# Performance work log

Measured on AMD Instinct MI355X. Metric: run time of the kernel, lower is better.

The kernel has to match this reference:

```python
import jax, jax.numpy as jnp
import numpy as np

N_NODES = 16384
N_EDGES = 524288
IN_CH = 128
HID_CH = 128
N_CLUST = 128


def _gcn_conv(x, W, b, src, dst, n):
    """PyG GCNConv: out = D^{-1/2} (A + I) D^{-1/2} (x @ W) + b, aggregating src -> dst."""
    h = x @ W  # [N, out]
    loop = jnp.arange(n)
    row = jnp.concatenate([src, loop])  # message sources (incl. self loops)
    col = jnp.concatenate([dst, loop])  # message targets
    deg = jax.ops.segment_sum(jnp.ones(row.shape, dtype=h.dtype), col, num_segments=n)
    dinv = jax.lax.rsqrt(deg)  # deg >= 1 thanks to self loops
    w = dinv[row] * dinv[col]  # [E + N]
    out = jax.ops.segment_sum(h[row] * w[:, None], col, num_segments=n)
    return out + b


def setup_inputs() -> dict:
    key = jax.random.key(0)
    k1, k2, k3, k4 = jax.random.split(key, 4)
    x = jax.random.normal(k1, (N_NODES, IN_CH), dtype=jnp.float32)
    edge_index = jax.random.randint(k2, (2, N_EDGES), 0, N_NODES, dtype=jnp.int64)
    W_emb = jax.random.normal(k3, (IN_CH, HID_CH), dtype=jnp.float32) / np.sqrt(IN_CH)
    b_emb = jnp.zeros((HID_CH,), dtype=jnp.float32)
    W_asn = jax.random.normal(k4, (IN_CH, N_CLUST), dtype=jnp.float32) / np.sqrt(IN_CH)
    b_asn = jnp.zeros((N_CLUST,), dtype=jnp.float32)
    return {"x": x, "edge_index": edge_index, "W_emb": W_emb, "b_emb": b_emb,
            "W_asn": W_asn, "b_asn": b_asn}


def reference(x, edge_index, W_emb, b_emb, W_asn, b_asn):
    n = x.shape[0]
    src, dst = edge_index[0], edge_index[1]
    x_emb = jax.nn.relu(_gcn_conv(x, W_emb, b_emb, src, dst, n))        # [N, H]
    S = jax.nn.softmax(_gcn_conv(x, W_asn, b_asn, src, dst, n), axis=-1)  # [N, K]
    x_pooled = S.T @ x_emb                                               # [K, H]
    A = jnp.zeros((n, n), dtype=x.dtype).at[src, dst].set(1.0)           # dense adjacency
    A_pooled = (S.T @ A) @ S                                             # [K, K]
    # torch code returns A_pooled.nonzero().T (dynamic shape, not jit-able);
    # we return the dense pooled adjacency carrying the same information.
    return x_pooled, A_pooled, S
```

## Files before the change

### kernel.cpp

```cpp
#include <hip/hip_runtime.h>

#define N_NODES 16384
#define N_EDGES 524288

typedef short bf16x8 __attribute__((ext_vector_type(8)));
typedef float f32x4 __attribute__((ext_vector_type(4)));

__device__ __forceinline__ ushort f2bf(float a) {
    uint u = __float_as_uint(a);
    return (ushort)((u + 0x7fff + ((u >> 16) & 1)) >> 16);
}
__device__ __forceinline__ uint pack2bf(float a, float b) {
    return (uint)f2bf(a) | ((uint)f2bf(b) << 16);
}
__device__ __forceinline__ float bflo(uint v) { return __uint_as_float(v << 16); }
__device__ __forceinline__ float bfhi(uint v) { return __uint_as_float(v & 0xffff0000u); }

__global__ void prep_kernel(uint4* __restrict__ count4, const float* __restrict__ W_emb,
                            const float* __restrict__ W_asn, ushort* __restrict__ wT) {
    int b = blockIdx.x;
    if (b < 16) { count4[b * 256 + threadIdx.x] = make_uint4(0, 0, 0, 0); return; }
    int idx = (b - 16) * 256 + threadIdx.x;
    int k = idx >> 8, n = idx & 255;
    float v = n < 128 ? W_emb[k * 128 + n] : W_asn[k * 128 + (n - 128)];
    wT[(size_t)n * 128 + k] = f2bf(v);
}

__global__ void hist_kernel(const int* __restrict__ dst, int* __restrict__ count) {
    int e = blockIdx.x * 256 + threadIdx.x;
    if (e < N_EDGES) atomicAdd(&count[dst[e]], 1);
}

__global__ void scan_kernel(const int* __restrict__ count, int* __restrict__ indptr,
                            int* __restrict__ cursor, float* __restrict__ dinv) {
    __shared__ int part[256];
    int t = threadIdx.x;
    int base = t * 64;
    int local[64];
    int s = 0;
#pragma unroll
    for (int i = 0; i < 64; ++i) { local[i] = s; s += count[base + i]; }
    part[t] = s;
    __syncthreads();
    for (int off = 1; off < 256; off <<= 1) {
        int v = (t >= off) ? part[t - off] : 0;
        __syncthreads();
        part[t] += v;
        __syncthreads();
    }
    int prefix = (t == 0) ? 0 : part[t - 1];
#pragma unroll
    for (int i = 0; i < 64; ++i) {
        int p = prefix + local[i];
        indptr[base + i] = p;
        cursor[base + i] = p;
        dinv[base + i] = rsqrtf((float)(count[base + i] + 1));
    }
    if (t == 255) indptr[N_NODES] = part[255];
}

__global__ void scatter_cvt_kernel(const int* __restrict__ src, const int* __restrict__ dst,
                                   int* __restrict__ cursor, int* __restrict__ sorted_src,
                                   const float* __restrict__ x, const float* __restrict__ dinv,
                                   ushort* __restrict__ x_bf) {
    int b = blockIdx.x;
    if (b < 2048) {
        int e = b * 256 + threadIdx.x;
        int d = dst[e];
        int p = atomicAdd(&cursor[d], 1);
        sorted_src[p] = src[e];
    } else {
        int i = (b - 2048) * 256 + threadIdx.x;
        float4 v = *(const float4*)(x + (size_t)i * 4);
        float dv = dinv[i >> 5];
        ushort4 o;
        o.x = f2bf(v.x * dv); o.y = f2bf(v.y * dv);
        o.z = f2bf(v.z * dv); o.w = f2bf(v.w * dv);
        *(ushort4*)(x_bf + (size_t)i * 4) = o;
    }
}

__global__ void agg_kernel(const uint* __restrict__ xp, const int* __restrict__ indptr,
                           const int* __restrict__ sorted_src, const float* __restrict__ dinv,
                           uint* __restrict__ agg) {
    int wv = threadIdx.x >> 6, lane = threadIdx.x & 63;
    int d = blockIdx.x * 4 + wv;
    int beg = indptr[d], end = indptr[d + 1];
    float ax = 0.f, ay = 0.f;
    for (int ch = beg; ch < end; ch += 64) {
        int take = end - ch; if (take > 64) take = 64;
        int myi = sorted_src[ch + (lane < take ? lane : 0)];
        int i = 0;
        for (; i + 4 <= take; i += 4) {
            int s0 = __shfl(myi, i),     s1 = __shfl(myi, i + 1);
            int s2 = __shfl(myi, i + 2), s3 = __shfl(myi, i + 3);
            uint v0 = xp[(size_t)s0 * 64 + lane];
            uint v1 = xp[(size_t)s1 * 64 + lane];
            uint v2 = xp[(size_t)s2 * 64 + lane];
            uint v3 = xp[(size_t)s3 * 64 + lane];
            ax += (bflo(v0) + bflo(v1)) + (bflo(v2) + bflo(v3));
            ay += (bfhi(v0) + bfhi(v1)) + (bfhi(v2) + bfhi(v3));
        }
        for (; i < take; ++i) {
            int s = __shfl(myi, i);
            uint v = xp[(size_t)s * 64 + lane];
            ax += bflo(v); ay += bfhi(v);
        }
    }
    uint vd = xp[(size_t)d * 64 + lane];
    ax += bflo(vd); ay += bfhi(vd);
    float di = dinv[d];
    agg[(size_t)d * 64 + lane] = pack2bf(ax * di, ay * di);
}

__global__ __launch_bounds__(512) void gemm_fused_mfma(
        const ushort* __restrict__ agg, const ushort* __restrict__ wT,
        const float* __restrict__ b_emb, const float* __restrict__ b_asn,
        float* __restrict__ S_out, uint* __restrict__ S_bf, uint* __restrict__ xe_bf) {
    __shared__ float hs[64][257];
    int l = threadIdx.x & 63, w = threadIdx.x >> 6;
    int lrow0 = (w >> 2) * 32;
    int m0 = blockIdx.x * 64 + lrow0;
    int n0 = (w & 3) * 64;
    int lr = l & 15, lk = (l >> 4) * 8;
    f32x4 acc[2][4] = {};
#pragma unroll
    for (int kk = 0; kk < 128; kk += 32) {
        bf16x8 a[2], b[4];
#pragma unroll
        for (int fm = 0; fm < 2; ++fm)
            a[fm] = *(const bf16x8*)(agg + (size_t)(m0 + fm * 16 + lr) * 128 + kk + lk);
#pragma unroll
        for (int fn = 0; fn < 4; ++fn)
            b[fn] = *(const bf16x8*)(wT + (size_t)(n0 + fn * 16 + lr) * 128 + kk + lk);
#pragma unroll
        for (int fm = 0; fm < 2; ++fm)
#pragma unroll
            for (int fn = 0; fn < 4; ++fn)
                acc[fm][fn] = __builtin_amdgcn_mfma_f32_16x16x32_bf16(
                    a[fm], b[fn], acc[fm][fn], 0, 0, 0);
    }
    int rbase = (l >> 4) * 4;
    const float* __restrict__ bvec = n0 < 128 ? b_emb : b_asn;
    int bcol0 = n0 & 127;
#pragma unroll
    for (int fn = 0; fn < 4; ++fn) {
        float bias = bvec[bcol0 + fn * 16 + lr];
#pragma unroll
        for (int fm = 0; fm < 2; ++fm)
#pragma unroll
            for (int r = 0; r < 4; ++r)
                hs[lrow0 + fm * 16 + rbase + r][n0 + fn * 16 + lr] = acc[fm][fn][r] + bias;
    }
    __syncthreads();
    int g = threadIdx.x >> 3, sub = threadIdx.x & 7;
    size_t grow = blockIdx.x * 64 + g;
    uint w8[8];
#pragma unroll
    for (int j = 0; j < 8; ++j) {
        float a0 = fmaxf(hs[g][sub * 16 + 2 * j], 0.f);
        float a1 = fmaxf(hs[g][sub * 16 + 2 * j + 1], 0.f);
        w8[j] = pack2bf(a0, a1);
    }
    *(uint4*)(&xe_bf[grow * 64 + sub * 8])     = make_uint4(w8[0], w8[1], w8[2], w8[3]);
    *(uint4*)(&xe_bf[grow * 64 + sub * 8 + 4]) = make_uint4(w8[4], w8[5], w8[6], w8[7]);
    float v[16];
#pragma unroll
    for (int j = 0; j < 16; ++j) v[j] = hs[g][128 + sub * 16 + j];
    float m = v[0];
#pragma unroll
    for (int j = 1; j < 16; ++j) m = fmaxf(m, v[j]);
    m = fmaxf(m, __shfl_xor(m, 1));
    m = fmaxf(m, __shfl_xor(m, 2));
    m = fmaxf(m, __shfl_xor(m, 4));
    float s = 0.f;
#pragma unroll
    for (int j = 0; j < 16; ++j) { v[j] = __expf(v[j] - m); s += v[j]; }
    s += __shfl_xor(s, 1);
    s += __shfl_xor(s, 2);
    s += __shfl_xor(s, 4);
    float inv = 1.f / s;
#pragma unroll
    for (int j = 0; j < 16; ++j) v[j] *= inv;
#pragma unroll
    for (int q = 0; q < 4; ++q)
        *(float4*)(&S_out[grow * 128 + sub * 16 + 4 * q]) =
            make_float4(v[4 * q], v[4 * q + 1], v[4 * q + 2], v[4 * q + 3]);
#pragma unroll
    for (int j = 0; j < 8; ++j) w8[j] = pack2bf(v[2 * j], v[2 * j + 1]);
    *(uint4*)(&S_bf[grow * 64 + sub * 8])     = make_uint4(w8[0], w8[1], w8[2], w8[3]);
    *(uint4*)(&S_bf[grow * 64 + sub * 8 + 4]) = make_uint4(w8[4], w8[5], w8[6], w8[7]);
}

__global__ void mt_kernel(const uint* __restrict__ S_bf, const int* __restrict__ indptr,
                          const int* __restrict__ sorted_src, uint* __restrict__ Mt_bf) {
    __shared__ int ss[4][1024];
    int wv = threadIdx.x >> 6, lane = threadIdx.x & 63;
    int d = blockIdx.x * 4 + wv;
    int beg = indptr[d];
    int len = indptr[d + 1] - beg;
    if (len > 1024) len = 1024;
    for (int i = lane; i < len; i += 64) ss[wv][i] = sorted_src[beg + i];
    __syncthreads();
    for (int i = lane; i < len; i += 64) {
        int s = ss[wv][i];
        for (int j = 0; j < i; ++j)
            if (ss[wv][j] == s) { ss[wv][i] = -1; break; }
    }
    __syncthreads();
    float ax = 0.f, ay = 0.f;
    for (int ch = 0; ch < len; ch += 64) {
        int take = len - ch; if (take > 64) take = 64;
        int myv = ss[wv][ch + (lane < take ? lane : 0)];
        int i = 0;
        for (; i + 4 <= take; i += 4) {
            int s0 = __shfl(myv, i),     s1 = __shfl(myv, i + 1);
            int s2 = __shfl(myv, i + 2), s3 = __shfl(myv, i + 3);
            float m0 = s0 >= 0 ? 1.f : 0.f, m1 = s1 >= 0 ? 1.f : 0.f;
            float m2 = s2 >= 0 ? 1.f : 0.f, m3 = s3 >= 0 ? 1.f : 0.f;
            uint v0 = S_bf[(size_t)(s0 >= 0 ? s0 : 0) * 64 + lane];
            uint v1 = S_bf[(size_t)(s1 >= 0 ? s1 : 0) * 64 + lane];
            uint v2 = S_bf[(size_t)(s2 >= 0 ? s2 : 0) * 64 + lane];
            uint v3 = S_bf[(size_t)(s3 >= 0 ? s3 : 0) * 64 + lane];
            ax += (bflo(v0) * m0 + bflo(v1) * m1) + (bflo(v2) * m2 + bflo(v3) * m3);
            ay += (bfhi(v0) * m0 + bfhi(v1) * m1) + (bfhi(v2) * m2 + bfhi(v3) * m3);
        }
        for (; i < take; ++i) {
            int s = __shfl(myv, i);
            if (s >= 0) {
                uint v = S_bf[(size_t)s * 64 + lane];
                ax += bflo(v); ay += bfhi(v);
            }
        }
    }
    Mt_bf[(size_t)d * 64 + lane] = pack2bf(ax, ay);
}

__global__ __launch_bounds__(256) void transpose_kernel(
        const ushort* __restrict__ S_bf, const ushort* __restrict__ xe_bf,
        const ushort* __restrict__ Mt_bf, ushort* __restrict__ S_T,
        ushort* __restrict__ xe_T, ushort* __restrict__ Mt_T) {
    __shared__ ushort tile[128][130];
    const ushort* __restrict__ src;
    ushort* __restrict__ dst;
    if (blockIdx.y == 0)      { src = S_bf;  dst = S_T; }
    else if (blockIdx.y == 1) { src = xe_bf; dst = xe_T; }
    else                      { src = Mt_bf; dst = Mt_T; }
    int tid = threadIdx.x;
    int n0 = blockIdx.x * 128;
    for (int i = tid; i < 2048; i += 256) {
        int r = i >> 4, c8 = (i & 15) << 3;
        const uint* p = (const uint*)(src + (size_t)(n0 + r) * 128 + c8);
        uint* t = (uint*)&tile[r][c8];
        t[0] = p[0]; t[1] = p[1]; t[2] = p[2]; t[3] = p[3];
    }
    __syncthreads();
    for (int i = tid; i < 2048; i += 256) {
        int ch = i >> 4, n8 = (i & 15) << 3;
        ushort v[8];
#pragma unroll
        for (int j = 0; j < 8; ++j) v[j] = tile[n8 + j][ch];
        uint4 o;
        o.x = (uint)v[0] | ((uint)v[1] << 16);
        o.y = (uint)v[2] | ((uint)v[3] << 16);
        o.z = (uint)v[4] | ((uint)v[5] << 16);
        o.w = (uint)v[6] | ((uint)v[7] << 16);
        *(uint4*)(dst + (size_t)ch * N_NODES + n0 + n8) = o;
    }
}

__global__ __launch_bounds__(512) void pool_stage1_mfma(
        const ushort* __restrict__ S_T, const ushort* __restrict__ xe_T,
        const ushort* __restrict__ Mt_T, float* __restrict__ part) {
    const ushort* __restrict__ A = blockIdx.y ? Mt_T : S_T;
    const ushort* __restrict__ B = blockIdx.y ? S_T : xe_T;
    float* __restrict__ out = part + (size_t)blockIdx.y * (64 * 16384) +
                              (size_t)blockIdx.x * 16384;
    int l = threadIdx.x & 63, w = threadIdx.x >> 6;
    int m0 = (w >> 2) * 64;
    int n0 = (w & 3) * 32;
    int lr = l & 15, lk = (l >> 4) * 8;
    int kb = blockIdx.x * 256;
    f32x4 acc[4][2] = {};
#pragma unroll 2
    for (int kk = 0; kk < 256; kk += 32) {
        bf16x8 a[4], b[2];
#pragma unroll
        for (int fm = 0; fm < 4; ++fm)
            a[fm] = *(const bf16x8*)(A + (size_t)(m0 + fm * 16 + lr) * N_NODES + kb + kk + lk);
#pragma unroll
        for (int fn = 0; fn < 2; ++fn)
            b[fn] = *(const bf16x8*)(B + (size_t)(n0 + fn * 16 + lr) * N_NODES + kb + kk + lk);
#pragma unroll
        for (int fm = 0; fm < 4; ++fm)
#pragma unroll
            for (int fn = 0; fn < 2; ++fn)
                acc[fm][fn] = __builtin_amdgcn_mfma_f32_16x16x32_bf16(
                    a[fm], b[fn], acc[fm][fn], 0, 0, 0);
    }
    int rbase = (l >> 4) * 4;
#pragma unroll
    for (int fm = 0; fm < 4; ++fm)
#pragma unroll
        for (int r = 0; r < 4; ++r)
#pragma unroll
            for (int fn = 0; fn < 2; ++fn)
                out[(size_t)(m0 + fm * 16 + rbase + r) * 128 + n0 + fn * 16 + lr] =
                    acc[fm][fn][r];
}

__global__ void pool_reduce_kernel(const float* __restrict__ part, float* __restrict__ out) {
    int idx = blockIdx.x * 256 + threadIdx.x;
    int g = idx >> 14;
    int o = idx & 16383;
    const float* __restrict__ p = part + (size_t)g * (64 * 16384) + o;
    float s = 0.f;
#pragma unroll 8
    for (int c = 0; c < 64; ++c) s += p[(size_t)c * 16384];
    out[idx] = s;
}

extern "C" void kernel_launch(void* const* d_in, const int* in_sizes, int n_in,
                              void* d_out, int out_size, void* d_ws, size_t ws_size,
                              hipStream_t stream) {
    const float* x      = (const float*)d_in[0];
    const int*   ei     = (const int*)d_in[1];
    const float* W_emb  = (const float*)d_in[2];
    const float* b_emb  = (const float*)d_in[3];
    const float* W_asn  = (const float*)d_in[4];
    const float* b_asn  = (const float*)d_in[5];
    const int* src = ei;
    const int* dst = ei + N_EDGES;

    float* out = (float*)d_out;
    float* S_out = out + 32768;

    char* ws = (char*)d_ws;
    ushort* x_bf   = (ushort*)(ws + 0);
    ushort* S_T    = (ushort*)(ws + 0);
    ushort* agg    = (ushort*)(ws + 4194304);
    ushort* xe_T   = (ushort*)(ws + 4194304);
    ushort* Mt_T   = (ushort*)(ws + 8388608);
    int*    sorted = (int*)   (ws + 12582912);
    ushort* wT     = (ushort*)(ws + 14680064);
    int*    count  = (int*)   (ws + 15204352);
    int*    indptr = (int*)   (ws + 15269888);
    int*    cursor = (int*)   (ws + 15400960);
    float*  dinv   = (float*) (ws + 15466496);
    uint*   S_bf   = (uint*)  (ws + 16777216);
    uint*   xe_bf  = (uint*)  (ws + 20971520);
    float*  part   = (float*) (ws + 16777216);
    uint*   Mt_bf  = (uint*)  (ws + 25165824);

    prep_kernel<<<144, 256, 0, stream>>>((uint4*)count, W_emb, W_asn, wT);
    hist_kernel<<<2048, 256, 0, stream>>>(dst, count);
    scan_kernel<<<1, 256, 0, stream>>>(count, indptr, cursor, dinv);
    scatter_cvt_kernel<<<4096, 256, 0, stream>>>(src, dst, cursor, sorted, x, dinv, x_bf);
    agg_kernel<<<4096, 256, 0, stream>>>((const uint*)x_bf, indptr, sorted, dinv, (uint*)agg);
    gemm_fused_mfma<<<256, 512, 0, stream>>>(agg, wT, b_emb, b_asn, S_out, S_bf, xe_bf);
    mt_kernel<<<4096, 256, 0, stream>>>(S_bf, indptr, sorted, Mt_bf);
    transpose_kernel<<<dim3(128, 3), 256, 0, stream>>>(
        (const ushort*)S_bf, (const ushort*)xe_bf, (const ushort*)Mt_bf, S_T, xe_T, Mt_T);
    pool_stage1_mfma<<<dim3(64, 2), 512, 0, stream>>>(S_T, xe_T, Mt_T, part);
    pool_reduce_kernel<<<128, 256, 0, stream>>>(part, out);
}
```

Measured before the change: 157.7 us.

## Gather two neighbor rows per wave with uint2 loads; fuse S/xe transpose into GEMM

The aggregation and Mt gather kernels now split each wave into two halves. Each half fetches a different neighbor row with 8-byte loads, and a cross-half shuffle reduces the partial sums at the end, so twice as many rows are in flight per load instruction. The GEMM epilogue writes ReLU'd embeddings and softmax assignments back to shared memory and stores the transposed bf16 xe_T and S_T directly. The transpose kernel now handles only Mt, which removes a round trip of the row-major xe/S buffers through global memory. The cost is the extra half-wave reduction and transposed global stores from the GEMM that are strided across node rows.

```diff
diff --git a/kernel.cpp b/kernel.cpp
--- a/kernel.cpp
+++ b/kernel.cpp
@@ -80,43 +80,61 @@
     }
 }
 
-__global__ void agg_kernel(const uint* __restrict__ xp, const int* __restrict__ indptr,
+__global__ void agg_kernel(const uint2* __restrict__ xp2, const int* __restrict__ indptr,
                            const int* __restrict__ sorted_src, const float* __restrict__ dinv,
-                           uint* __restrict__ agg) {
+                           uint2* __restrict__ agg2) {
     int wv = threadIdx.x >> 6, lane = threadIdx.x & 63;
     int d = blockIdx.x * 4 + wv;
     int beg = indptr[d], end = indptr[d + 1];
-    float ax = 0.f, ay = 0.f;
+    int half = lane >> 5, hl = lane & 31;
+    float a0 = 0.f, a1 = 0.f, a2 = 0.f, a3 = 0.f;
     for (int ch = beg; ch < end; ch += 64) {
         int take = end - ch; if (take > 64) take = 64;
         int myi = sorted_src[ch + (lane < take ? lane : 0)];
         int i = 0;
-        for (; i + 4 <= take; i += 4) {
-            int s0 = __shfl(myi, i),     s1 = __shfl(myi, i + 1);
-            int s2 = __shfl(myi, i + 2), s3 = __shfl(myi, i + 3);
-            uint v0 = xp[(size_t)s0 * 64 + lane];
-            uint v1 = xp[(size_t)s1 * 64 + lane];
-            uint v2 = xp[(size_t)s2 * 64 + lane];
-            uint v3 = xp[(size_t)s3 * 64 + lane];
-            ax += (bflo(v0) + bflo(v1)) + (bflo(v2) + bflo(v3));
-            ay += (bfhi(v0) + bfhi(v1)) + (bfhi(v2) + bfhi(v3));
-        }
-        for (; i < take; ++i) {
+        for (; i + 8 <= take; i += 8) {
+            int s0 = __shfl(myi, i + half);
+            int s1 = __shfl(myi, i + 2 + half);
+            int s2 = __shfl(myi, i + 4 + half);
+            int s3 = __shfl(myi, i + 6 + half);
+            uint2 v0 = xp2[(size_t)s0 * 32 + hl];
+            uint2 v1 = xp2[(size_t)s1 * 32 + hl];
+            uint2 v2 = xp2[(size_t)s2 * 32 + hl];
+            uint2 v3 = xp2[(size_t)s3 * 32 + hl];
+            a0 += (bflo(v0.x) + bflo(v1.x)) + (bflo(v2.x) + bflo(v3.x));
+            a1 += (bfhi(v0.x) + bfhi(v1.x)) + (bfhi(v2.x) + bfhi(v3.x));
+            a2 += (bflo(v0.y) + bflo(v1.y)) + (bflo(v2.y) + bflo(v3.y));
+            a3 += (bfhi(v0.y) + bfhi(v1.y)) + (bfhi(v2.y) + bfhi(v3.y));
+        }
+        for (; i + 2 <= take; i += 2) {
+            int s = __shfl(myi, i + half);
+            uint2 v = xp2[(size_t)s * 32 + hl];
+            a0 += bflo(v.x); a1 += bfhi(v.x); a2 += bflo(v.y); a3 += bfhi(v.y);
+        }
+        if (i < take) {
             int s = __shfl(myi, i);
-            uint v = xp[(size_t)s * 64 + lane];
-            ax += bflo(v); ay += bfhi(v);
-        }
-    }
-    uint vd = xp[(size_t)d * 64 + lane];
-    ax += bflo(vd); ay += bfhi(vd);
-    float di = dinv[d];
-    agg[(size_t)d * 64 + lane] = pack2bf(ax * di, ay * di);
+            if (half == 0) {
+                uint2 v = xp2[(size_t)s * 32 + hl];
+                a0 += bflo(v.x); a1 += bfhi(v.x); a2 += bflo(v.y); a3 += bfhi(v.y);
+            }
+        }
+    }
+    a0 += __shfl_xor(a0, 32); a1 += __shfl_xor(a1, 32);
+    a2 += __shfl_xor(a2, 32); a3 += __shfl_xor(a3, 32);
+    if (half == 0) {
+        uint2 vd = xp2[(size_t)d * 32 + hl];
+        a0 += bflo(vd.x); a1 += bfhi(vd.x); a2 += bflo(vd.y); a3 += bfhi(vd.y);
+        float di = dinv[d];
+        uint2 o; o.x = pack2bf(a0 * di, a1 * di); o.y = pack2bf(a2 * di, a3 * di);
+        agg2[(size_t)d * 32 + hl] = o;
+    }
 }
 
 __global__ __launch_bounds__(512) void gemm_fused_mfma(
         const ushort* __restrict__ agg, const ushort* __restrict__ wT,
         const float* __restrict__ b_emb, const float* __restrict__ b_asn,
-        float* __restrict__ S_out, uint* __restrict__ S_bf, uint* __restrict__ xe_bf) {
+        float* __restrict__ S_out, uint* __restrict__ S_bf,
+        ushort* __restrict__ xe_T, ushort* __restrict__ S_T) {
     __shared__ float hs[64][257];
     int l = threadIdx.x & 63, w = threadIdx.x >> 6;
     int lrow0 = (w >> 2) * 32;
@@ -155,15 +173,11 @@
     __syncthreads();
     int g = threadIdx.x >> 3, sub = threadIdx.x & 7;
     size_t grow = blockIdx.x * 64 + g;
-    uint w8[8];
-#pragma unroll
-    for (int j = 0; j < 8; ++j) {
-        float a0 = fmaxf(hs[g][sub * 16 + 2 * j], 0.f);
-        float a1 = fmaxf(hs[g][sub * 16 + 2 * j + 1], 0.f);
-        w8[j] = pack2bf(a0, a1);
-    }
-    *(uint4*)(&xe_bf[grow * 64 + sub * 8])     = make_uint4(w8[0], w8[1], w8[2], w8[3]);
-    *(uint4*)(&xe_bf[grow * 64 + sub * 8 + 4]) = make_uint4(w8[4], w8[5], w8[6], w8[7]);
+#pragma unroll
+    for (int j = 0; j < 16; ++j) {
+        float a0 = fmaxf(hs[g][sub * 16 + j], 0.f);
+        hs[g][sub * 16 + j] = a0;
+    }
     float v[16];
 #pragma unroll
     for (int j = 0; j < 16; ++j) v[j] = hs[g][128 + sub * 16 + j];
@@ -180,8 +194,9 @@
     s += __shfl_xor(s, 2);
     s += __shfl_xor(s, 4);
     float inv = 1.f / s;
-#pragma unroll
-    for (int j = 0; j < 16; ++j) v[j] *= inv;
+    uint w8[8];
+#pragma unroll
+    for (int j = 0; j < 16; ++j) { v[j] *= inv; hs[g][128 + sub * 16 + j] = v[j]; }
 #pragma unroll
     for (int q = 0; q < 4; ++q)
         *(float4*)(&S_out[grow * 128 + sub * 16 + 4 * q]) =
@@ -190,10 +205,27 @@
     for (int j = 0; j < 8; ++j) w8[j] = pack2bf(v[2 * j], v[2 * j + 1]);
     *(uint4*)(&S_bf[grow * 64 + sub * 8])     = make_uint4(w8[0], w8[1], w8[2], w8[3]);
     *(uint4*)(&S_bf[grow * 64 + sub * 8 + 4]) = make_uint4(w8[4], w8[5], w8[6], w8[7]);
-}
-
-__global__ void mt_kernel(const uint* __restrict__ S_bf, const int* __restrict__ indptr,
-                          const int* __restrict__ sorted_src, uint* __restrict__ Mt_bf) {
+    __syncthreads();
+    int brow = blockIdx.x * 64;
+#pragma unroll
+    for (int r = 0; r < 4; ++r) {
+        int c = (threadIdx.x >> 3) + 64 * r;
+        int oct = threadIdx.x & 7;
+        uint w4[4];
+#pragma unroll
+        for (int q = 0; q < 4; ++q) {
+            float u0 = hs[oct * 8 + 2 * q][c];
+            float u1 = hs[oct * 8 + 2 * q + 1][c];
+            w4[q] = pack2bf(u0, u1);
+        }
+        ushort* __restrict__ T = c < 128 ? xe_T : S_T;
+        *(uint4*)(&T[(size_t)(c & 127) * N_NODES + brow + oct * 8]) =
+            make_uint4(w4[0], w4[1], w4[2], w4[3]);
+    }
+}
+
+__global__ void mt_kernel(const uint2* __restrict__ Sp2, const int* __restrict__ indptr,
+                          const int* __restrict__ sorted_src, uint2* __restrict__ Mt2) {
     __shared__ int ss[4][1024];
     int wv = threadIdx.x >> 6, lane = threadIdx.x & 63;
     int d = blockIdx.x * 4 + wv;
@@ -208,49 +240,59 @@
             if (ss[wv][j] == s) { ss[wv][i] = -1; break; }
     }
     __syncthreads();
-    float ax = 0.f, ay = 0.f;
+    int half = lane >> 5, hl = lane & 31;
+    float a0 = 0.f, a1 = 0.f, a2 = 0.f, a3 = 0.f;
     for (int ch = 0; ch < len; ch += 64) {
         int take = len - ch; if (take > 64) take = 64;
         int myv = ss[wv][ch + (lane < take ? lane : 0)];
         int i = 0;
-        for (; i + 4 <= take; i += 4) {
-            int s0 = __shfl(myv, i),     s1 = __shfl(myv, i + 1);
-            int s2 = __shfl(myv, i + 2), s3 = __shfl(myv, i + 3);
+        for (; i + 8 <= take; i += 8) {
+            int s0 = __shfl(myv, i + half);
+            int s1 = __shfl(myv, i + 2 + half);
+            int s2 = __shfl(myv, i + 4 + half);
+            int s3 = __shfl(myv, i + 6 + half);
             float m0 = s0 >= 0 ? 1.f : 0.f, m1 = s1 >= 0 ? 1.f : 0.f;
             float m2 = s2 >= 0 ? 1.f : 0.f, m3 = s3 >= 0 ? 1.f : 0.f;
-            uint v0 = S_bf[(size_t)(s0 >= 0 ? s0 : 0) * 64 + lane];
-            uint v1 = S_bf[(size_t)(s1 >= 0 ? s1 : 0) * 64 + lane];
-            uint v2 = S_bf[(size_t)(s2 >= 0 ? s2 : 0) * 64 + lane];
-            uint v3 = S_bf[(size_t)(s3 >= 0 ? s3 : 0) * 64 + lane];
-            ax += (bflo(v0) * m0 + bflo(v1) * m1) + (bflo(v2) * m2 + bflo(v3) * m3);
-            ay += (bfhi(v0) * m0 + bfhi(v1) * m1) + (bfhi(v2) * m2 + bfhi(v3) * m3);
-        }
-        for (; i < take; ++i) {
+            uint2 v0 = Sp2[(size_t)(s0 >= 0 ? s0 : 0) * 32 + hl];
+            uint2 v1 = Sp2[(size_t)(s1 >= 0 ? s1 : 0) * 32 + hl];
+            uint2 v2 = Sp2[(size_t)(s2 >= 0 ? s2 : 0) * 32 + hl];
+            uint2 v3 = Sp2[(size_t)(s3 >= 0 ? s3 : 0) * 32 + hl];
+            a0 += (bflo(v0.x) * m0 + bflo(v1.x) * m1) + (bflo(v2.x) * m2 + bflo(v3.x) * m3);
+            a1 += (bfhi(v0.x) * m0 + bfhi(v1.x) * m1) + (bfhi(v2.x) * m2 + bfhi(v3.x) * m3);
+            a2 += (bflo(v0.y) * m0 + bflo(v1.y) * m1) + (bflo(v2.y) * m2 + bflo(v3.y) * m3);
+            a3 += (bfhi(v0.y) * m0 + bfhi(v1.y) * m1) + (bfhi(v2.y) * m2 + bfhi(v3.y) * m3);
+        }
+        for (; i + 2 <= take; i += 2) {
+            int s = __shfl(myv, i + half);
+            if (s >= 0) {
+                uint2 v = Sp2[(size_t)s * 32 + hl];
+                a0 += bflo(v.x); a1 += bfhi(v.x); a2 += bflo(v.y); a3 += bfhi(v.y);
+            }
+        }
+        if (i < take) {
             int s = __shfl(myv, i);
-            if (s >= 0) {
-                uint v = S_bf[(size_t)s * 64 + lane];
-                ax += bflo(v); ay += bfhi(v);
+            if (half == 0 && s >= 0) {
+                uint2 v = Sp2[(size_t)s * 32 + hl];
+                a0 += bflo(v.x); a1 += bfhi(v.x); a2 += bflo(v.y); a3 += bfhi(v.y);
             }
         }
     }
-    Mt_bf[(size_t)d * 64 + lane] = pack2bf(ax, ay);
+    a0 += __shfl_xor(a0, 32); a1 += __shfl_xor(a1, 32);
+    a2 += __shfl_xor(a2, 32); a3 += __shfl_xor(a3, 32);
+    if (half == 0) {
+        uint2 o; o.x = pack2bf(a0, a1); o.y = pack2bf(a2, a3);
+        Mt2[(size_t)d * 32 + hl] = o;
+    }
 }
 
 __global__ __launch_bounds__(256) void transpose_kernel(
-        const ushort* __restrict__ S_bf, const ushort* __restrict__ xe_bf,
-        const ushort* __restrict__ Mt_bf, ushort* __restrict__ S_T,
-        ushort* __restrict__ xe_T, ushort* __restrict__ Mt_T) {
+        const ushort* __restrict__ Mt_bf, ushort* __restrict__ Mt_T) {
     __shared__ ushort tile[128][130];
-    const ushort* __restrict__ src;
-    ushort* __restrict__ dst;
-    if (blockIdx.y == 0)      { src = S_bf;  dst = S_T; }
-    else if (blockIdx.y == 1) { src = xe_bf; dst = xe_T; }
-    else                      { src = Mt_bf; dst = Mt_T; }
     int tid = threadIdx.x;
     int n0 = blockIdx.x * 128;
     for (int i = tid; i < 2048; i += 256) {
         int r = i >> 4, c8 = (i & 15) << 3;
-        const uint* p = (const uint*)(src + (size_t)(n0 + r) * 128 + c8);
+        const uint* p = (const uint*)(Mt_bf + (size_t)(n0 + r) * 128 + c8);
         uint* t = (uint*)&tile[r][c8];
         t[0] = p[0]; t[1] = p[1]; t[2] = p[2]; t[3] = p[3];
     }
@@ -265,7 +307,7 @@
         o.y = (uint)v[2] | ((uint)v[3] << 16);
         o.z = (uint)v[4] | ((uint)v[5] << 16);
         o.w = (uint)v[6] | ((uint)v[7] << 16);
-        *(uint4*)(dst + (size_t)ch * N_NODES + n0 + n8) = o;
+        *(uint4*)(Mt_T + (size_t)ch * N_NODES + n0 + n8) = o;
     }
 }
 
@@ -339,8 +381,8 @@
     ushort* x_bf   = (ushort*)(ws + 0);
     ushort* S_T    = (ushort*)(ws + 0);
     ushort* agg    = (ushort*)(ws + 4194304);
-    ushort* xe_T   = (ushort*)(ws + 4194304);
-    ushort* Mt_T   = (ushort*)(ws + 8388608);
+    ushort* Mt_T   = (ushort*)(ws + 4194304);
+    ushort* xe_T   = (ushort*)(ws + 8388608);
     int*    sorted = (int*)   (ws + 12582912);
     ushort* wT     = (ushort*)(ws + 14680064);
     int*    count  = (int*)   (ws + 15204352);
@@ -348,19 +390,18 @@
     int*    cursor = (int*)   (ws + 15400960);
     float*  dinv   = (float*) (ws + 15466496);
     uint*   S_bf   = (uint*)  (ws + 16777216);
-    uint*   xe_bf  = (uint*)  (ws + 20971520);
+    uint*   Mt_bf  = (uint*)  (ws + 20971520);
     float*  part   = (float*) (ws + 16777216);
-    uint*   Mt_bf  = (uint*)  (ws + 25165824);
 
     prep_kernel<<<144, 256, 0, stream>>>((uint4*)count, W_emb, W_asn, wT);
     hist_kernel<<<2048, 256, 0, stream>>>(dst, count);
     scan_kernel<<<1, 256, 0, stream>>>(count, indptr, cursor, dinv);
     scatter_cvt_kernel<<<4096, 256, 0, stream>>>(src, dst, cursor, sorted, x, dinv, x_bf);
-    agg_kernel<<<4096, 256, 0, stream>>>((const uint*)x_bf, indptr, sorted, dinv, (uint*)agg);
-    gemm_fused_mfma<<<256, 512, 0, stream>>>(agg, wT, b_emb, b_asn, S_out, S_bf, xe_bf);
-    mt_kernel<<<4096, 256, 0, stream>>>(S_bf, indptr, sorted, Mt_bf);
-    transpose_kernel<<<dim3(128, 3), 256, 0, stream>>>(
-        (const ushort*)S_bf, (const ushort*)xe_bf, (const ushort*)Mt_bf, S_T, xe_T, Mt_T);
+    agg_kernel<<<4096, 256, 0, stream>>>((const uint2*)x_bf, indptr, sorted, dinv,
+                                         (uint2*)agg);
+    gemm_fused_mfma<<<256, 512, 0, stream>>>(agg, wT, b_emb, b_asn, S_out, S_bf, xe_T, S_T);
+    mt_kernel<<<4096, 256, 0, stream>>>((const uint2*)S_bf, indptr, sorted, (uint2*)Mt_bf);
+    transpose_kernel<<<128, 256, 0, stream>>>((const ushort*)Mt_bf, Mt_T);
     pool_stage1_mfma<<<dim3(64, 2), 512, 0, stream>>>(S_T, xe_T, Mt_T, part);
     pool_reduce_kernel<<<128, 256, 0, stream>>>(part, out);
 }
```

Result: no change. 158.4 us (+0.5%).
